# Performance work log

Measured on AMD Instinct MI355X. Metric: run time of the kernel, lower is better.

The kernel has to match this reference:

```python
import jax, jax.numpy as jnp
import numpy as np


def setup_inputs() -> dict:
    key = jax.random.key(0)
    ks = jax.random.split(key, 4)
    B, C, H, W = 8, 256, 64, 64
    x = jax.random.normal(ks[0], (B, C, H, W), dtype=jnp.float32)
    Wq = jax.random.normal(ks[1], (C, C), dtype=jnp.float32) * 0.02
    Wk = jax.random.normal(ks[2], (C, C), dtype=jnp.float32) * 0.02
    Wv = jax.random.normal(ks[3], (C, C), dtype=jnp.float32) * 0.02
    bq = jnp.zeros((C,), dtype=jnp.float32)
    bk = jnp.zeros((C,), dtype=jnp.float32)
    bv = jnp.zeros((C,), dtype=jnp.float32)
    gamma = jnp.float32(0.5)  # learned scalar (torch init is 0.0; nonzero here for a nontrivial output)
    return {"x": x, "Wq": Wq, "bq": bq, "Wk": Wk, "bk": bk, "Wv": Wv, "bv": bv, "gamma": gamma}


def reference(x, Wq, bq, Wk, bk, Wv, bv, gamma):
    B, C, H, W = x.shape
    N = H * W
    f = x.reshape(B, C, N)  # flatten spatial tokens
    # 1x1 Conv1d == per-token linear: out[b,d,n] = sum_c W[d,c] * f[b,c,n] + b[d]
    q = jnp.einsum('dc,bcn->bdn', Wq, f) + bq[:, None]  # [B, C, N]
    k = jnp.einsum('dc,bcn->bdn', Wk, f) + bk[:, None]  # [B, C, N]
    v = jnp.einsum('dc,bcn->bdn', Wv, f) + bv[:, None]  # [B, C, N]
    # query_key[b, n, m] = sum_c q[b,c,n] * k[b,c,m], divided by width W (shape[-1], NOT N)
    qk = jnp.einsum('bcn,bcm->bnm', q, k) / W  # [B, N, N]
    # softmax over dim=1 => over the QUERY-token axis (SAGAN quirk)
    attn = jax.nn.softmax(qk, axis=1)
    # out[b,c,m] = sum_n v[b,c,n] * attn[b,n,m]
    o = jnp.einsum('bcn,bnm->bcm', v, attn).reshape(B, C, H, W)
    return gamma * o + x
```

## Files before the change

### kernel.cpp

```cpp
#include <hip/hip_runtime.h>

typedef __bf16 bf16_t;
typedef __bf16 bf16x8 __attribute__((ext_vector_type(8)));
typedef float f32x16 __attribute__((ext_vector_type(16)));
typedef float f32x4 __attribute__((ext_vector_type(4)));

#define NB 8
#define NC 256
#define NN 4096

__device__ __forceinline__ f32x16 mfma32(bf16x8 a, bf16x8 b, f32x16 c) {
  return __builtin_amdgcn_mfma_f32_32x32x16_bf16(a, b, c, 0, 0, 0);
}

__device__ __forceinline__ f32x4 mfma16(uint2 a, uint2 b, f32x4 c) {
  union { uint2 u; long long l; } A, B;
  A.u = a; B.u = b;
  return __builtin_amdgcn_mfma_f32_16x16x32_fp8_fp8(A.l, B.l, c, 0, 0, 0);
}

__device__ __forceinline__ void gload_lds16(const void* g, void* l) {
  __builtin_amdgcn_global_load_lds((const __attribute__((address_space(1))) void*)g,
                                   (__attribute__((address_space(3))) void*)l, 16, 0, 0);
}

__device__ __forceinline__ unsigned int packbf2(float lo, float hi) {
  union { bf16_t h; unsigned short s; } a, b;
  a.h = (bf16_t)lo; b.h = (bf16_t)hi;
  return (unsigned int)a.s | ((unsigned int)b.s << 16);
}

__device__ __forceinline__ f32x16 fzero() {
  f32x16 z;
#pragma unroll
  for (int r = 0; r < 16; r++) z[r] = 0.f;
  return z;
}

#define QSCALE (0.015625f * 1.44269504088896f)

__global__ void kconv_w(const float* __restrict__ Wq, const float* __restrict__ bq,
                        const float* __restrict__ Wk, const float* __restrict__ bk,
                        const float* __restrict__ Wv, const float* __restrict__ bv,
                        bf16_t* __restrict__ Wc, float* __restrict__ bc) {
  int idx = blockIdx.x * 256 + threadIdx.x;
  int d = idx >> 8;
  float w;
  if (d < 256)      w = Wq[idx];
  else if (d < 512) w = Wk[idx - 65536];
  else              w = Wv[idx - 131072];
  Wc[idx] = (bf16_t)w;
  if (idx < 768) {
    float v = idx < 256 ? bq[idx] : (idx < 512 ? bk[idx - 256] : bv[idx - 512]);
    bc[idx] = v;
  }
}

__global__ void ktranspose(const float* __restrict__ x, bf16_t* __restrict__ fT) {
  __shared__ float tile[64][65];
  int bid = blockIdx.x;
  int b = bid >> 8;
  int r = bid & 255;
  int n0 = (r >> 2) * 64;
  int c0 = (r & 3) * 64;
  int t = threadIdx.x;
  const float* xb = x + ((long)b * NC + c0) * NN + n0;
  int lr = t >> 4;
  int lc = (t & 15) * 4;
#pragma unroll
  for (int i = 0; i < 4; i++) {
    float4 v4 = *(const float4*)(xb + (long)(lr + i * 16) * NN + lc);
    tile[lr + i * 16][lc + 0] = v4.x; tile[lr + i * 16][lc + 1] = v4.y;
    tile[lr + i * 16][lc + 2] = v4.z; tile[lr + i * 16][lc + 3] = v4.w;
  }
  __syncthreads();
  int nl = t >> 2;
  int cc = (t & 3) * 16;
  bf16_t* dst = fT + ((long)b * NN + n0 + nl) * NC + c0 + cc;
  union { bf16_t h[8]; uint4 u; } p0, p1;
#pragma unroll
  for (int j = 0; j < 8; j++) p0.h[j] = (bf16_t)tile[cc + j][nl];
#pragma unroll
  for (int j = 0; j < 8; j++) p1.h[j] = (bf16_t)tile[cc + 8 + j][nl];
  *(uint4*)dst = p0.u;
  *(uint4*)(dst + 8) = p1.u;
}

__global__ __launch_bounds__(256) void kproj(const bf16_t* __restrict__ Wc, const float* __restrict__ bc,
                                             const bf16_t* __restrict__ fT,
                                             unsigned char* __restrict__ qT8, unsigned char* __restrict__ kT8,
                                             unsigned char* __restrict__ vO8) {
  __shared__ bf16_t ft[128 * 256];
  int bid = blockIdx.x;
  int mt = bid % 6;
  int nb = bid / 6;
  int d0 = mt * 128;
  int gc0 = nb * 128;
  int b = gc0 >> 12;
  int n0 = gc0 & 4095;
  int t = threadIdx.x, lane = t & 63, w = t >> 6;
  int lm = lane & 31, g = lane >> 5;
  const bf16_t* ftb = fT + ((long)b * NN + n0) * NC;
#pragma unroll
  for (int i2 = 0; i2 < 16; i2++) {
    int call = w * 16 + i2;
    int p = call * 1024 + lane * 16;
    int n = p >> 9, cb = p & 511;
    int scb = cb ^ ((n & 7) << 4);
    gload_lds16(ftb + (long)n * NC + (scb >> 1), (char*)ft + call * 1024);
  }
  __syncthreads();

  f32x16 acc00 = fzero(), acc01 = fzero(), acc10 = fzero(), acc11 = fzero();
  int dbase = d0 + (w >> 1) * 64;
  int nbase = (w & 1) * 64;
  const bf16_t* wr = Wc + (long)dbase * NC;
#pragma unroll
  for (int j = 0; j < 16; j++) {
    int cc = j * 16 + g * 8;
    bf16x8 a0 = *(const bf16x8*)(wr + (long)lm * NC + cc);
    bf16x8 a1 = *(const bf16x8*)(wr + (long)(lm + 32) * NC + cc);
    int row0 = nbase + lm;
    bf16x8 b0 = *(const bf16x8*)((char*)ft + row0 * 512 + ((cc * 2) ^ ((row0 & 7) << 4)));
    int row1 = row0 + 32;
    bf16x8 b1 = *(const bf16x8*)((char*)ft + row1 * 512 + ((cc * 2) ^ ((row1 & 7) << 4)));
    acc00 = mfma32(a0, b0, acc00);
    acc01 = mfma32(a0, b1, acc01);
    acc10 = mfma32(a1, b0, acc10);
    acc11 = mfma32(a1, b1, acc11);
  }

  auto epi = [&](f32x16 a, int dt, int nt2) {
    int db = dbase + dt * 32;
    int colg = n0 + nbase + nt2 * 32 + lm;
    long tb = ((long)b * 128 + (colg >> 5)) * 8192;
    int n5 = colg & 31;
    if (mt >= 4) {
      int q5 = (n5 >> 2) & 3;
      int e5 = ((n5 >> 4) << 2) + (n5 & 3);
      int ct0 = (db - 512) >> 4;
#pragma unroll
      for (int r = 0; r < 16; r++) {
        int d = db + (r & 3) + 8 * (r >> 2) + 4 * g;
        int ct = ct0 + (r >> 3);
        int kq = (r & 3) + 8 * ((r >> 2) & 1) + 4 * g;
        unsigned int f8 = __builtin_amdgcn_cvt_pk_fp8_f32(a[r] + bc[d], 0.f, 0, false);
        vO8[tb + (ct * 64 + q5 * 16 + kq) * 8 + e5] = (unsigned char)f8;
      }
    } else if (mt < 2) {
      int h = (n5 >> 4) & 1;
      int nr = n5 & 15;
      int j = db >> 5;
#pragma unroll
      for (int t4 = 0; t4 < 4; t4++) {
        int cb = db + 8 * t4 + 4 * g;
        unsigned int pk = __builtin_amdgcn_cvt_pk_fp8_f32(a[4 * t4 + 0] + bc[cb + 0],
                                                          a[4 * t4 + 1] + bc[cb + 1], 0, false);
        pk = __builtin_amdgcn_cvt_pk_fp8_f32(a[4 * t4 + 2] + bc[cb + 2],
                                             a[4 * t4 + 3] + bc[cb + 3], pk, true);
        *(unsigned int*)(qT8 + tb + (j * 2 + h) * 512 + (t4 * 16 + nr) * 8 + 4 * g) = pk;
      }
    } else {
      unsigned char* dst = kT8 + ((long)b * NN + colg) * 256 - 256;
#pragma unroll
      for (int r2 = 0; r2 < 8; r2++) {
        int r = r2 * 2;
        int d = db + (r & 3) + 8 * (r >> 2) + 4 * g;
        unsigned int pk = __builtin_amdgcn_cvt_pk_fp8_f32(a[r] + bc[d], a[r + 1] + bc[d + 1], 0, false);
        *(unsigned short*)(dst + d) = (unsigned short)pk;
      }
    }
  };
  epi(acc00, 0, 0); epi(acc01, 0, 1); epi(acc10, 1, 0); epi(acc11, 1, 1);
}

__global__ __launch_bounds__(512, 4) void kattn(const unsigned char* __restrict__ qT8,
                                                const unsigned char* __restrict__ kT8,
                                                const unsigned char* __restrict__ vO8,
                                                char* __restrict__ R0, char* __restrict__ R1, int iters) {
  __shared__ unsigned char Kt[2][8192];
  __shared__ unsigned char Vt[2][8192];
  int bid = blockIdx.x;
  int b = bid & 7;
  int mtile = (bid >> 3) & 31;
  int split = bid >> 8;
  int nt0 = split * iters, ntE = nt0 + iters;
  int t = threadIdx.x, lane = t & 63, w = t >> 6;
  int l4 = lane & 15, q = (lane >> 4) & 3;
  int mw = mtile * 128 + w * 16;
  const unsigned char* qb = qT8 + (long)b * 1048576;
  const unsigned char* vtb = vO8 + (long)b * 1048576;

  uint2 qf[8];
  const unsigned char* kb = kT8 + ((long)b * NN + mw + l4) * 256 + q * 8;
#pragma unroll
  for (int j = 0; j < 8; j++) qf[j] = *(const uint2*)(kb + j * 32);

  f32x4 acc[16];
#pragma unroll
  for (int ct = 0; ct < 16; ct++) acc[ct] = f32x4{0.f, 0.f, 0.f, 0.f};
  float lsum = 0.f;

  auto stageK = [&](int nt, int bufi) {
    gload_lds16(qb + (long)nt * 8192 + w * 1024 + lane * 16, &Kt[bufi][w * 1024]);
  };
  auto stageV = [&](int nt, int bufi) {
    gload_lds16(vtb + (long)nt * 8192 + w * 1024 + lane * 16, &Vt[bufi][w * 1024]);
  };

  stageK(nt0, 0);
  stageV(nt0, 0);
  __syncthreads();

  int buf = 0;
  for (int nt = nt0; nt < ntE; nt++) {
    bool more = nt + 1 < ntE;
    if (more) { stageK(nt + 1, buf ^ 1); stageV(nt + 1, buf ^ 1); }
    __builtin_amdgcn_s_setprio(1);
    const unsigned char* kbase = &Kt[buf][0] + lane * 8;
    f32x4 s0 = f32x4{0.f, 0.f, 0.f, 0.f}, s1 = f32x4{0.f, 0.f, 0.f, 0.f};
#pragma unroll
    for (int j = 0; j < 8; j++) {
      uint2 a0 = *(const uint2*)(kbase + (2 * j) * 512);
      s0 = mfma16(a0, qf[j], s0);
      uint2 a1 = *(const uint2*)(kbase + (2 * j + 1) * 512);
      s1 = mfma16(a1, qf[j], s1);
    }
    __builtin_amdgcn_s_setprio(0);
    float e[8];
#pragma unroll
    for (int r = 0; r < 4; r++) {
      e[r] = __builtin_amdgcn_exp2f(s0[r] * QSCALE);
      e[4 + r] = __builtin_amdgcn_exp2f(s1[r] * QSCALE);
    }
    lsum += ((e[0] + e[1]) + (e[2] + e[3])) + ((e[4] + e[5]) + (e[6] + e[7]));
    uint2 pf;
    pf.x = __builtin_amdgcn_cvt_pk_fp8_f32(e[0], e[1], 0, false);
    pf.x = __builtin_amdgcn_cvt_pk_fp8_f32(e[2], e[3], pf.x, true);
    pf.y = __builtin_amdgcn_cvt_pk_fp8_f32(e[4], e[5], 0, false);
    pf.y = __builtin_amdgcn_cvt_pk_fp8_f32(e[6], e[7], pf.y, true);
    __builtin_amdgcn_s_setprio(1);
    const unsigned char* vbase = &Vt[buf][0] + lane * 8;
#pragma unroll
    for (int ct = 0; ct < 16; ct++) {
      uint2 va = *(const uint2*)(vbase + ct * 512);
      acc[ct] = mfma16(va, pf, acc[ct]);
    }
    __builtin_amdgcn_s_setprio(0);
    __syncthreads();
    buf ^= 1;
  }
  float ltot = lsum + __shfl_xor(lsum, 16, 64);
  ltot += __shfl_xor(ltot, 32, 64);
  char* R = split ? R1 : R0;
  unsigned int* PP = (unsigned int*)R;
  float* MLf = (float*)(R + 16777216);
  int mg = ((b * 32 + mtile) << 3) + w;
  if (lane < 16) MLf[mg * 16 + lane] = ltot;
#pragma unroll
  for (int ct = 0; ct < 16; ct++) {
    uint2 pk;
    pk.x = packbf2(acc[ct][0], acc[ct][1]);
    pk.y = packbf2(acc[ct][2], acc[ct][3]);
    *(uint2*)(PP + (mg * 16 + ct) * 128 + lane * 2) = pk;
  }
}

__global__ __launch_bounds__(256) void kcombine(const char* __restrict__ R0, const char* __restrict__ R1,
                                                int nsplit, const float* __restrict__ x,
                                                const float* __restrict__ gma, float* __restrict__ out) {
  int tid = blockIdx.x * 256 + threadIdx.x;
  const unsigned int* P0 = (const unsigned int*)R0;
  const float* ML0 = (const float*)(R0 + 16777216);
  int mg = tid >> 11;
  int ct = (tid >> 7) & 15;
  int lane = (tid >> 1) & 63;
  int rr = tid & 1;
  int b = mg >> 8, mtile = (mg >> 3) & 31, w = mg & 7;
  int m = mtile * 128 + w * 16 + (lane & 15);
  int c0 = ct * 16 + ((lane >> 4) & 3) * 4 + rr * 2;
  unsigned int p0 = P0[tid];
  float ox = __uint_as_float(p0 << 16);
  float oy = __uint_as_float(p0 & 0xffff0000u);
  float L = ML0[mg * 16 + (lane & 15)];
  if (nsplit == 2) {
    const unsigned int* P1 = (const unsigned int*)R1;
    const float* ML1 = (const float*)(R1 + 16777216);
    unsigned int p1 = P1[tid];
    ox += __uint_as_float(p1 << 16);
    oy += __uint_as_float(p1 & 0xffff0000u);
    L += ML1[mg * 16 + (lane & 15)];
  }
  float sc = gma[0] / L;
  long o0 = ((long)(b * NC + c0)) * NN + m;
  out[o0] = ox * sc + x[o0];
  out[o0 + NN] = oy * sc + x[o0 + NN];
}

extern "C" void kernel_launch(void* const* d_in, const int* in_sizes, int n_in,
                              void* d_out, int out_size, void* d_ws, size_t ws_size,
                              hipStream_t stream) {
  const float* x   = (const float*)d_in[0];
  const float* Wq  = (const float*)d_in[1];
  const float* bq  = (const float*)d_in[2];
  const float* Wk  = (const float*)d_in[3];
  const float* bk  = (const float*)d_in[4];
  const float* Wv  = (const float*)d_in[5];
  const float* bv  = (const float*)d_in[6];
  const float* gma = (const float*)d_in[7];
  float* out = (float*)d_out;
  char* ws = (char*)d_ws;
  unsigned char* qT8 = (unsigned char*)(ws);
  unsigned char* kT8 = (unsigned char*)(ws + 8388608);
  unsigned char* vO8 = (unsigned char*)(ws + 16777216);
  bf16_t* fT = (bf16_t*)(ws + 25165824);
  bf16_t* Wc = (bf16_t*)(ws + 41943040);
  float*  bc = (float*)(ws + 42336256);
  char* R0 = ws + 25165824;
  char* R1 = ws + 42340352;
  size_t need2 = 42340352 + 16908288;
  int nsplit = (ws_size >= need2) ? 2 : 1;

  kconv_w<<<768, 256, 0, stream>>>(Wq, bq, Wk, bk, Wv, bv, Wc, bc);
  ktranspose<<<2048, 256, 0, stream>>>(x, fT);
  kproj<<<1536, 256, 0, stream>>>(Wc, bc, fT, qT8, kT8, vO8);
  kattn<<<256 * nsplit, 512, 0, stream>>>(qT8, kT8, vO8, R0, R1, 128 / nsplit);
  kcombine<<<16384, 256, 0, stream>>>(R0, R1, nsplit, x, gma, out);
}
```

Measured before the change: 180.3 us.

## Switch attention MFMAs to 16x16x128 scaled fp8 with relaid-out Q/V tiles

Replaces the 16x16x32 fp8 MFMAs in the attention kernel with the MI355 16x16x128 f8f6f4 scaled MFMA, using unit scales. The projection epilogue is changed to write Q and V in a new fragment layout to match. V is now staged in 128-token super-tiles (32 KB per buffer), so the PV product runs once per four score sub-tiles. This cuts MFMA instruction count and LDS read overhead, but quadruples V LDS use to 80 KB total, which may lower occupancy below the launch-bounds target.

```diff
diff --git a/kernel.cpp b/kernel.cpp
--- a/kernel.cpp
+++ b/kernel.cpp
@@ -4,6 +4,7 @@
 typedef __bf16 bf16x8 __attribute__((ext_vector_type(8)));
 typedef float f32x16 __attribute__((ext_vector_type(16)));
 typedef float f32x4 __attribute__((ext_vector_type(4)));
+typedef int i32x8 __attribute__((ext_vector_type(8)));
 
 #define NB 8
 #define NC 256
@@ -13,10 +14,9 @@
   return __builtin_amdgcn_mfma_f32_32x32x16_bf16(a, b, c, 0, 0, 0);
 }
 
-__device__ __forceinline__ f32x4 mfma16(uint2 a, uint2 b, f32x4 c) {
-  union { uint2 u; long long l; } A, B;
-  A.u = a; B.u = b;
-  return __builtin_amdgcn_mfma_f32_16x16x32_fp8_fp8(A.l, B.l, c, 0, 0, 0);
+__device__ __forceinline__ f32x4 mfma128(i32x8 a, i32x8 b, f32x4 c) {
+  return __builtin_amdgcn_mfma_scale_f32_16x16x128_f8f6f4(
+      a, b, c, 0, 0, 0, 0x7f7f7f7f, 0, 0x7f7f7f7f);
 }
 
 __device__ __forceinline__ void gload_lds16(const void* g, void* l) {
@@ -133,24 +133,24 @@
   auto epi = [&](f32x16 a, int dt, int nt2) {
     int db = dbase + dt * 32;
     int colg = n0 + nbase + nt2 * 32 + lm;
-    long tb = ((long)b * 128 + (colg >> 5)) * 8192;
-    int n5 = colg & 31;
     if (mt >= 4) {
-      int q5 = (n5 >> 2) & 3;
-      int e5 = ((n5 >> 4) << 2) + (n5 & 3);
-      int ct0 = (db - 512) >> 4;
+      int nn = colg & 127;
+      long base = ((long)b * 32 + (colg >> 7)) * 32768 +
+                  ((nn >> 6) & 1) * 1024 + 16 * ((nn >> 2) & 3) * 16 +
+                  4 * ((nn >> 4) & 3) + (nn & 3);
 #pragma unroll
       for (int r = 0; r < 16; r++) {
         int d = db + (r & 3) + 8 * (r >> 2) + 4 * g;
-        int ct = ct0 + (r >> 3);
-        int kq = (r & 3) + 8 * ((r >> 2) & 1) + 4 * g;
+        int c = d - 512;
         unsigned int f8 = __builtin_amdgcn_cvt_pk_fp8_f32(a[r] + bc[d], 0.f, 0, false);
-        vO8[tb + (ct * 64 + q5 * 16 + kq) * 8 + e5] = (unsigned char)f8;
+        vO8[base + (c >> 4) * 2048 + (c & 15) * 16] = (unsigned char)f8;
       }
     } else if (mt < 2) {
-      int h = (n5 >> 4) & 1;
-      int nr = n5 & 15;
-      int j = db >> 5;
+      long tb = ((long)b * 128 + (colg >> 5)) * 8192;
+      int h = (colg >> 4) & 1;
+      int l = (colg & 15) + 16 * ((db >> 5) & 3);
+      int cc = db >> 7;
+      long ob = tb + (2 * h + cc) * 2048 + l * 16;
 #pragma unroll
       for (int t4 = 0; t4 < 4; t4++) {
         int cb = db + 8 * t4 + 4 * g;
@@ -158,7 +158,7 @@
                                                           a[4 * t4 + 1] + bc[cb + 1], 0, false);
         pk = __builtin_amdgcn_cvt_pk_fp8_f32(a[4 * t4 + 2] + bc[cb + 2],
                                              a[4 * t4 + 3] + bc[cb + 3], pk, true);
-        *(unsigned int*)(qT8 + tb + (j * 2 + h) * 512 + (t4 * 16 + nr) * 8 + 4 * g) = pk;
+        *(unsigned int*)(qT8 + ob + (t4 >> 1) * 1024 + 8 * (t4 & 1) + 4 * g) = pk;
       }
     } else {
       unsigned char* dst = kT8 + ((long)b * NN + colg) * 256 - 256;
@@ -177,78 +177,97 @@
 __global__ __launch_bounds__(512, 4) void kattn(const unsigned char* __restrict__ qT8,
                                                 const unsigned char* __restrict__ kT8,
                                                 const unsigned char* __restrict__ vO8,
-                                                char* __restrict__ R0, char* __restrict__ R1, int iters) {
+                                                char* __restrict__ R0, char* __restrict__ R1, int nss) {
   __shared__ unsigned char Kt[2][8192];
-  __shared__ unsigned char Vt[2][8192];
+  __shared__ unsigned char Vs[2][32768];
   int bid = blockIdx.x;
   int b = bid & 7;
   int mtile = (bid >> 3) & 31;
   int split = bid >> 8;
-  int nt0 = split * iters, ntE = nt0 + iters;
   int t = threadIdx.x, lane = t & 63, w = t >> 6;
   int l4 = lane & 15, q = (lane >> 4) & 3;
   int mw = mtile * 128 + w * 16;
   const unsigned char* qb = qT8 + (long)b * 1048576;
   const unsigned char* vtb = vO8 + (long)b * 1048576;
-
-  uint2 qf[8];
-  const unsigned char* kb = kT8 + ((long)b * NN + mw + l4) * 256 + q * 8;
-#pragma unroll
-  for (int j = 0; j < 8; j++) qf[j] = *(const uint2*)(kb + j * 32);
+  int sub0 = split * nss * 4;
+  int sup0 = split * nss;
+
+  i32x8 qf0, qf1;
+  {
+    const unsigned char* kb = kT8 + ((long)b * NN + mw + l4) * 256 + q * 32;
+    union { uint4 u[2]; i32x8 v; } r;
+    r.u[0] = *(const uint4*)(kb);      r.u[1] = *(const uint4*)(kb + 16);
+    qf0 = r.v;
+    r.u[0] = *(const uint4*)(kb + 128); r.u[1] = *(const uint4*)(kb + 144);
+    qf1 = r.v;
+  }
 
   f32x4 acc[16];
 #pragma unroll
   for (int ct = 0; ct < 16; ct++) acc[ct] = f32x4{0.f, 0.f, 0.f, 0.f};
   float lsum = 0.f;
-
-  auto stageK = [&](int nt, int bufi) {
-    gload_lds16(qb + (long)nt * 8192 + w * 1024 + lane * 16, &Kt[bufi][w * 1024]);
+  unsigned int pf[8];
+
+  auto stageK = [&](int gi, int bufi) {
+    gload_lds16(qb + (long)gi * 8192 + t * 16, &Kt[bufi][t * 16]);
   };
-  auto stageV = [&](int nt, int bufi) {
-    gload_lds16(vtb + (long)nt * 8192 + w * 1024 + lane * 16, &Vt[bufi][w * 1024]);
+  auto stageVp = [&](int gs, int bufi, int part) {
+    gload_lds16(vtb + (long)gs * 32768 + part * 8192 + t * 16,
+                &Vs[bufi][part * 8192 + t * 16]);
   };
-
-  stageK(nt0, 0);
-  stageV(nt0, 0);
+  auto ldfrag = [&](const unsigned char* fb) {
+    union { uint4 u[2]; i32x8 v; } r;
+    r.u[0] = *(const uint4*)(fb + lane * 16);
+    r.u[1] = *(const uint4*)(fb + 1024 + lane * 16);
+    return r.v;
+  };
+
+  stageK(sub0, 0);
+#pragma unroll
+  for (int p = 0; p < 4; p++) stageVp(sup0, 0, p);
   __syncthreads();
 
-  int buf = 0;
-  for (int nt = nt0; nt < ntE; nt++) {
-    bool more = nt + 1 < ntE;
-    if (more) { stageK(nt + 1, buf ^ 1); stageV(nt + 1, buf ^ 1); }
-    __builtin_amdgcn_s_setprio(1);
-    const unsigned char* kbase = &Kt[buf][0] + lane * 8;
-    f32x4 s0 = f32x4{0.f, 0.f, 0.f, 0.f}, s1 = f32x4{0.f, 0.f, 0.f, 0.f};
-#pragma unroll
-    for (int j = 0; j < 8; j++) {
-      uint2 a0 = *(const uint2*)(kbase + (2 * j) * 512);
-      s0 = mfma16(a0, qf[j], s0);
-      uint2 a1 = *(const uint2*)(kbase + (2 * j + 1) * 512);
-      s1 = mfma16(a1, qf[j], s1);
+#pragma unroll 1
+  for (int s = 0; s < nss; s++) {
+    int snext = sup0 + (s + 1 < nss ? s + 1 : s);
+    int sbuf = s & 1;
+#pragma unroll
+    for (int tt = 0; tt < 4; tt++) {
+      int li = 4 * s + tt;
+      if (li + 1 < 4 * nss) stageK(sub0 + li + 1, (tt & 1) ^ 1);
+      stageVp(snext, sbuf ^ 1, tt);
+      __builtin_amdgcn_s_setprio(1);
+      const unsigned char* kbase = &Kt[tt & 1][0];
+      f32x4 s0 = f32x4{0.f, 0.f, 0.f, 0.f}, s1 = f32x4{0.f, 0.f, 0.f, 0.f};
+      s0 = mfma128(ldfrag(kbase), qf0, s0);
+      s0 = mfma128(ldfrag(kbase + 2048), qf1, s0);
+      s1 = mfma128(ldfrag(kbase + 4096), qf0, s1);
+      s1 = mfma128(ldfrag(kbase + 6144), qf1, s1);
+      __builtin_amdgcn_s_setprio(0);
+      float e0[4], e1[4];
+#pragma unroll
+      for (int r = 0; r < 4; r++) {
+        e0[r] = __builtin_amdgcn_exp2f(s0[r] * QSCALE);
+        e1[r] = __builtin_amdgcn_exp2f(s1[r] * QSCALE);
+      }
+      lsum += ((e0[0] + e0[1]) + (e0[2] + e0[3])) + ((e1[0] + e1[1]) + (e1[2] + e1[3]));
+      unsigned int u0 = __builtin_amdgcn_cvt_pk_fp8_f32(e0[0], e0[1], 0, false);
+      pf[2 * tt] = __builtin_amdgcn_cvt_pk_fp8_f32(e0[2], e0[3], u0, true);
+      unsigned int u1 = __builtin_amdgcn_cvt_pk_fp8_f32(e1[0], e1[1], 0, false);
+      pf[2 * tt + 1] = __builtin_amdgcn_cvt_pk_fp8_f32(e1[2], e1[3], u1, true);
+      if (tt == 3) {
+        union { unsigned int u[8]; i32x8 v; } pB;
+#pragma unroll
+        for (int j = 0; j < 8; j++) pB.u[j] = pf[j];
+        __builtin_amdgcn_s_setprio(1);
+        const unsigned char* vbase = &Vs[sbuf][0];
+#pragma unroll
+        for (int ct = 0; ct < 16; ct++)
+          acc[ct] = mfma128(ldfrag(vbase + ct * 2048), pB.v, acc[ct]);
+        __builtin_amdgcn_s_setprio(0);
+      }
+      __syncthreads();
     }
-    __builtin_amdgcn_s_setprio(0);
-    float e[8];
-#pragma unroll
-    for (int r = 0; r < 4; r++) {
-      e[r] = __builtin_amdgcn_exp2f(s0[r] * QSCALE);
-      e[4 + r] = __builtin_amdgcn_exp2f(s1[r] * QSCALE);
-    }
-    lsum += ((e[0] + e[1]) + (e[2] + e[3])) + ((e[4] + e[5]) + (e[6] + e[7]));
-    uint2 pf;
-    pf.x = __builtin_amdgcn_cvt_pk_fp8_f32(e[0], e[1], 0, false);
-    pf.x = __builtin_amdgcn_cvt_pk_fp8_f32(e[2], e[3], pf.x, true);
-    pf.y = __builtin_amdgcn_cvt_pk_fp8_f32(e[4], e[5], 0, false);
-    pf.y = __builtin_amdgcn_cvt_pk_fp8_f32(e[6], e[7], pf.y, true);
-    __builtin_amdgcn_s_setprio(1);
-    const unsigned char* vbase = &Vt[buf][0] + lane * 8;
-#pragma unroll
-    for (int ct = 0; ct < 16; ct++) {
-      uint2 va = *(const uint2*)(vbase + ct * 512);
-      acc[ct] = mfma16(va, pf, acc[ct]);
-    }
-    __builtin_amdgcn_s_setprio(0);
-    __syncthreads();
-    buf ^= 1;
   }
   float ltot = lsum + __shfl_xor(lsum, 16, 64);
   ltot += __shfl_xor(ltot, 32, 64);
@@ -324,6 +343,6 @@
   kconv_w<<<768, 256, 0, stream>>>(Wq, bq, Wk, bk, Wv, bv, Wc, bc);
   ktranspose<<<2048, 256, 0, stream>>>(x, fT);
   kproj<<<1536, 256, 0, stream>>>(Wc, bc, fT, qT8, kT8, vO8);
-  kattn<<<256 * nsplit, 512, 0, stream>>>(qT8, kT8, vO8, R0, R1, 128 / nsplit);
+  kattn<<<256 * nsplit, 512, 0, stream>>>(qT8, kT8, vO8, R0, R1, 32 / nsplit);
   kcombine<<<16384, 256, 0, stream>>>(R0, R1, nsplit, x, gma, out);
 }
```

Measured after the change: 532.0 us. +195.2%, slower.

## Process two K/V tiles per barrier with four-slot LDS ring; reorder kproj block mapping

Applied to the files above, without the earlier changes.

The attention loop now stages two tiles ahead into a four-slot LDS ring and computes two tiles between each __syncthreads, halving barrier count. It also remaps kproj block indices so consecutive blocks share the same weight tile. The larger LDS footprint (64KB vs 32KB) may reduce occupancy against the launch bound of 4 blocks, and the loop assumes iters is even.

```diff
diff --git a/kernel.cpp b/kernel.cpp
--- a/kernel.cpp
+++ b/kernel.cpp
@@ -92,8 +92,8 @@
                                              unsigned char* __restrict__ vO8) {
   __shared__ bf16_t ft[128 * 256];
   int bid = blockIdx.x;
-  int mt = bid % 6;
-  int nb = bid / 6;
+  int mt = bid >> 8;
+  int nb = bid & 255;
   int d0 = mt * 128;
   int gc0 = nb * 128;
   int b = gc0 >> 12;
@@ -178,13 +178,13 @@
                                                 const unsigned char* __restrict__ kT8,
                                                 const unsigned char* __restrict__ vO8,
                                                 char* __restrict__ R0, char* __restrict__ R1, int iters) {
-  __shared__ unsigned char Kt[2][8192];
-  __shared__ unsigned char Vt[2][8192];
+  __shared__ unsigned char Kt[4][8192];
+  __shared__ unsigned char Vt[4][8192];
   int bid = blockIdx.x;
   int b = bid & 7;
   int mtile = (bid >> 3) & 31;
   int split = bid >> 8;
-  int nt0 = split * iters, ntE = nt0 + iters;
+  int nt0 = split * iters;
   int t = threadIdx.x, lane = t & 63, w = t >> 6;
   int l4 = lane & 15, q = (lane >> 4) & 3;
   int mw = mtile * 128 + w * 16;
@@ -201,23 +201,15 @@
   for (int ct = 0; ct < 16; ct++) acc[ct] = f32x4{0.f, 0.f, 0.f, 0.f};
   float lsum = 0.f;
 
-  auto stageK = [&](int nt, int bufi) {
-    gload_lds16(qb + (long)nt * 8192 + w * 1024 + lane * 16, &Kt[bufi][w * 1024]);
+  auto stageK = [&](int nt, int slot) {
+    gload_lds16(qb + (long)(nt0 + nt) * 8192 + w * 1024 + lane * 16, &Kt[slot][w * 1024]);
   };
-  auto stageV = [&](int nt, int bufi) {
-    gload_lds16(vtb + (long)nt * 8192 + w * 1024 + lane * 16, &Vt[bufi][w * 1024]);
+  auto stageV = [&](int nt, int slot) {
+    gload_lds16(vtb + (long)(nt0 + nt) * 8192 + w * 1024 + lane * 16, &Vt[slot][w * 1024]);
   };
-
-  stageK(nt0, 0);
-  stageV(nt0, 0);
-  __syncthreads();
-
-  int buf = 0;
-  for (int nt = nt0; nt < ntE; nt++) {
-    bool more = nt + 1 < ntE;
-    if (more) { stageK(nt + 1, buf ^ 1); stageV(nt + 1, buf ^ 1); }
+  auto tilework = [&](int slot) {
     __builtin_amdgcn_s_setprio(1);
-    const unsigned char* kbase = &Kt[buf][0] + lane * 8;
+    const unsigned char* kbase = &Kt[slot][0] + lane * 8;
     f32x4 s0 = f32x4{0.f, 0.f, 0.f, 0.f}, s1 = f32x4{0.f, 0.f, 0.f, 0.f};
 #pragma unroll
     for (int j = 0; j < 8; j++) {
@@ -240,15 +232,28 @@
     pf.y = __builtin_amdgcn_cvt_pk_fp8_f32(e[4], e[5], 0, false);
     pf.y = __builtin_amdgcn_cvt_pk_fp8_f32(e[6], e[7], pf.y, true);
     __builtin_amdgcn_s_setprio(1);
-    const unsigned char* vbase = &Vt[buf][0] + lane * 8;
+    const unsigned char* vbase = &Vt[slot][0] + lane * 8;
 #pragma unroll
     for (int ct = 0; ct < 16; ct++) {
       uint2 va = *(const uint2*)(vbase + ct * 512);
       acc[ct] = mfma16(va, pf, acc[ct]);
     }
     __builtin_amdgcn_s_setprio(0);
+  };
+
+  stageK(0, 0); stageV(0, 0);
+  stageK(1, 1); stageV(1, 1);
+  __syncthreads();
+
+#pragma unroll 1
+  for (int s = 0; s < iters; s += 2) {
+    if (s + 2 < iters) {
+      stageK(s + 2, (s + 2) & 3); stageV(s + 2, (s + 2) & 3);
+      stageK(s + 3, (s + 3) & 3); stageV(s + 3, (s + 3) & 3);
+    }
+    tilework(s & 3);
+    tilework((s + 1) & 3);
     __syncthreads();
-    buf ^= 1;
   }
   float ltot = lsum + __shfl_xor(lsum, 16, 64);
   ltot += __shfl_xor(ltot, 32, 64);
```

After: 287.9 us. 1.6x slower.
